# Kernel optimization log

Hardware: AMD Instinct MI355X
Metric: run time of the kernel (lower is better)

## Reference

```python
import jax, jax.numpy as jnp
import numpy as np

N_NODES = 50000
N_EDGES = 800000
D = 128


def setup_inputs() -> dict:
    key = jax.random.key(0)
    k1, k2, k3, k4, k5 = jax.random.split(key, 5)
    feature = jax.random.normal(k1, (N_NODES, D), dtype=jnp.float32)
    src = jax.random.randint(k2, (N_EDGES,), 0, N_NODES, dtype=jnp.int64)
    dst = jax.random.randint(k3, (N_EDGES,), 0, N_NODES, dtype=jnp.int64)
    # Linear(in_feats=128, out_feats=128) params
    W = jax.random.normal(k4, (D, D), dtype=jnp.float32) * (1.0 / np.sqrt(D))
    b = jax.random.normal(k5, (D,), dtype=jnp.float32) * 0.01
    return {"feature": feature, "src": src, "dst": dst, "W": W, "b": b}


def reference(feature, src, dst, W, b):
    n = feature.shape[0]
    # copy_src message: each edge carries h[src]; segment-mean over in-edges at dst
    msgs = feature[src]                                      # [E, D] irregular gather
    summed = jax.ops.segment_sum(msgs, dst, num_segments=n)  # [N, D] scatter-add
    cnt = jax.ops.segment_sum(jnp.ones((src.shape[0],), dtype=feature.dtype),
                              dst, num_segments=n)           # in-degree per node
    h = summed / jnp.clip(cnt, 1.0)[:, None]                 # mean (isolated nodes -> 0)
    # NodeApplyModule: ReLU(W h + b)
    return jax.nn.relu(h @ W.T + b)
```

## Files before the change

kernel.cpp:

```cpp
#include <hip/hip_runtime.h>

#define NN 50000
#define NE 800000
#define DD 128
#define NPAD 50176
#define NSB 49
#define WGB 512
#define HBW 391
#define HB 782


#define ACC4(A, V) { A.x += V.x; A.y += V.y; A.z += V.z; A.w += V.w; }

#define BSUM_PREFIX(bsum, sbase)                                   \
  {                                                                \
    int tt = threadIdx.x;                                          \
    if (tt < 64) {                                                 \
      int b = (tt < NSB) ? bsum[tt] : 0;                           \
      int z = b;                                                   \
      _Pragma("unroll") for (int o = 1; o < 64; o <<= 1) {         \
        int w_ = __shfl_up(z, o);                                  \
        if (tt >= o) z += w_;                                      \
      }                                                            \
      sbase[tt] = z - b;                                           \
    }                                                              \
    __syncthreads();                                               \
  }

__global__ __launch_bounds__(256) void k_gemm_hist(
    const float* __restrict__ feat, const float* __restrict__ W,
    float* __restrict__ g, const int* __restrict__ dst, int* __restrict__ cnt) {
  __shared__ float4 Wc4[DD * 32];
  __shared__ float hs[4][8][DD];
  int tid = threadIdx.x;
  int bid = blockIdx.x;

  if (bid >= WGB) {
    int idx = (bid - WGB) * 256 + tid;
    if (idx < NE / 8) {
      const int4* d4 = (const int4*)dst;
      int4 a = d4[idx * 2];
      int4 b = d4[idx * 2 + 1];
      atomicAdd(&cnt[a.x], 1); atomicAdd(&cnt[a.y], 1);
      atomicAdd(&cnt[a.z], 1); atomicAdd(&cnt[a.w], 1);
      atomicAdd(&cnt[b.x], 1); atomicAdd(&cnt[b.y], 1);
      atomicAdd(&cnt[b.z], 1); atomicAdd(&cnt[b.w], 1);
    }
    return;
  }

  {
    const float4* W4 = (const float4*)W;
#pragma unroll
    for (int i = 0; i < 16; ++i) {
      int fidx = tid + (i << 8);
      int c = fidx >> 5, kq = fidx & 31;
      Wc4[c * 32 + (kq ^ (c & 31))] = W4[fidx];
    }
  }
  __syncthreads();

  int w = tid >> 6, lane = tid & 63;
  int s = lane & 31;
  const float2* feat2 = (const float2*)feat;

  for (int gid = bid * 4 + w; gid < NN / 8; gid += WGB * 4) {
    int r0 = gid * 8;
#pragma unroll
    for (int r = 0; r < 8; ++r) {
      float2 v = feat2[(size_t)(r0 + r) * 64 + lane];
      hs[w][r][lane * 2] = v.x;
      hs[w][r][lane * 2 + 1] = v.y;
    }
    float2 acc[8] = {};
#pragma unroll 2
    for (int kc = 0; kc < 32; ++kc) {
      float4 w0 = Wc4[lane * 32 + (kc ^ s)];
      float4 w1 = Wc4[(lane + 64) * 32 + (kc ^ s)];
#pragma unroll
      for (int r = 0; r < 8; ++r) {
        float4 h = *(const float4*)&hs[w][r][kc * 4];
        acc[r].x += h.x * w0.x; acc[r].x += h.y * w0.y;
        acc[r].x += h.z * w0.z; acc[r].x += h.w * w0.w;
        acc[r].y += h.x * w1.x; acc[r].y += h.y * w1.y;
        acc[r].y += h.z * w1.z; acc[r].y += h.w * w1.w;
      }
    }
#pragma unroll
    for (int r = 0; r < 8; ++r) {
      g[(size_t)(r0 + r) * DD + lane] = acc[r].x;
      g[(size_t)(r0 + r) * DD + lane + 64] = acc[r].y;
    }
  }
}

__global__ __launch_bounds__(1024) void k_scan(const int* __restrict__ cnt,
                                               int* __restrict__ pos,
                                               int* __restrict__ bsum) {
  __shared__ int wsum[16];
  int t = threadIdx.x;
  int gidx = blockIdx.x * 1024 + t;
  int v = cnt[gidx];
  int x = v;
#pragma unroll
  for (int o = 1; o < 64; o <<= 1) {
    int y = __shfl_up(x, o);
    if ((t & 63) >= o) x += y;
  }
  if ((t & 63) == 63) wsum[t >> 6] = x;
  __syncthreads();
  if (t < 64) {
    int y = (t < 16) ? wsum[t] : 0;
    int z = y;
#pragma unroll
    for (int o = 1; o < 16; o <<= 1) {
      int w = __shfl_up(z, o);
      if (t >= o) z += w;
    }
    if (t < 16) wsum[t] = z - y;
  }
  __syncthreads();
  pos[gidx] = wsum[t >> 6] + x - v;
  if (t == 1023) bsum[blockIdx.x] = wsum[15] + x;
}

__global__ __launch_bounds__(256) void k_fill(const int* __restrict__ src,
                                              const int* __restrict__ dst,
                                              int* __restrict__ pos,
                                              int* __restrict__ csr,
                                              const int* __restrict__ bsum) {
  __shared__ int sbase[64];
  BSUM_PREFIX(bsum, sbase)
  int idx = blockIdx.x * 256 + threadIdx.x;
  if (idx < NE / 4) {
    int4 d = ((const int4*)dst)[idx];
    int4 s = ((const int4*)src)[idx];
    int p;
    p = atomicAdd(&pos[d.x], 1); csr[sbase[d.x >> 10] + p] = s.x;
    p = atomicAdd(&pos[d.y], 1); csr[sbase[d.y >> 10] + p] = s.y;
    p = atomicAdd(&pos[d.z], 1); csr[sbase[d.z >> 10] + p] = s.z;
    p = atomicAdd(&pos[d.w], 1); csr[sbase[d.w >> 10] + p] = s.w;
  }
}

__global__ __launch_bounds__(256) void k_gmean(const float* __restrict__ g,
                                               const int* __restrict__ csr,
                                               const int* __restrict__ pos,
                                               const int* __restrict__ cnt,
                                               const int* __restrict__ bsum,
                                               const float* __restrict__ bias,
                                               float* __restrict__ out) {
  __shared__ int sbase[64];
  BSUM_PREFIX(bsum, sbase)
  int tid = threadIdx.x;
  int hw = tid >> 5, l32 = tid & 31;
  int n = blockIdx.x * 8 + hw;
  int c = cnt[n];
  int endg = sbase[n >> 10] + pos[n];
  int start = endg - c;
  float4 a0 = make_float4(0.f, 0.f, 0.f, 0.f), a1 = a0, a2 = a0, a3 = a0;

  for (int base = start; base < endg; base += 32) {
    int m = endg - base;
    if (m > 32) m = 32;
    int s = (l32 < m) ? csr[base + l32] : 0;
    int j = 0;
    for (; j + 8 <= m; j += 8) {
      int s0 = __shfl(s, j + 0, 32), s1 = __shfl(s, j + 1, 32),
          s2 = __shfl(s, j + 2, 32), s3 = __shfl(s, j + 3, 32),
          s4 = __shfl(s, j + 4, 32), s5 = __shfl(s, j + 5, 32),
          s6 = __shfl(s, j + 6, 32), s7 = __shfl(s, j + 7, 32);
      float4 v0 = ((const float4*)(g + (size_t)s0 * DD))[l32];
      float4 v1 = ((const float4*)(g + (size_t)s1 * DD))[l32];
      float4 v2 = ((const float4*)(g + (size_t)s2 * DD))[l32];
      float4 v3 = ((const float4*)(g + (size_t)s3 * DD))[l32];
      float4 v4 = ((const float4*)(g + (size_t)s4 * DD))[l32];
      float4 v5 = ((const float4*)(g + (size_t)s5 * DD))[l32];
      float4 v6 = ((const float4*)(g + (size_t)s6 * DD))[l32];
      float4 v7 = ((const float4*)(g + (size_t)s7 * DD))[l32];
      ACC4(a0, v0) ACC4(a1, v1) ACC4(a2, v2) ACC4(a3, v3)
      ACC4(a0, v4) ACC4(a1, v5) ACC4(a2, v6) ACC4(a3, v7)
    }
    for (; j < m; ++j) {
      int sj = __shfl(s, j, 32);
      float4 v = ((const float4*)(g + (size_t)sj * DD))[l32];
      ACC4(a0, v)
    }
  }
  a0.x += a1.x + a2.x + a3.x;
  a0.y += a1.y + a2.y + a3.y;
  a0.z += a1.z + a2.z + a3.z;
  a0.w += a1.w + a2.w + a3.w;
  float inv = 1.0f / fmaxf((float)c, 1.0f);
  float4 b4 = ((const float4*)bias)[l32];
  float4 o;
  o.x = fmaxf(a0.x * inv + b4.x, 0.f);
  o.y = fmaxf(a0.y * inv + b4.y, 0.f);
  o.z = fmaxf(a0.z * inv + b4.z, 0.f);
  o.w = fmaxf(a0.w * inv + b4.w, 0.f);
  ((float4*)(out + (size_t)n * DD))[l32] = o;
}

__global__ __launch_bounds__(128) void k_hist(const int* __restrict__ dst,
                                              int* __restrict__ cnt) {
  int idx = blockIdx.x * 128 + threadIdx.x;
  if (idx < NE / 8) {
    const int4* d4 = (const int4*)dst;
    int4 a = d4[idx * 2];
    int4 b = d4[idx * 2 + 1];
    atomicAdd(&cnt[a.x], 1); atomicAdd(&cnt[a.y], 1);
    atomicAdd(&cnt[a.z], 1); atomicAdd(&cnt[a.w], 1);
    atomicAdd(&cnt[b.x], 1); atomicAdd(&cnt[b.y], 1);
    atomicAdd(&cnt[b.z], 1); atomicAdd(&cnt[b.w], 1);
  }
}

__global__ __launch_bounds__(256) void k_gsum(const float* __restrict__ feat,
                                              const int* __restrict__ csr,
                                              const int* __restrict__ pos,
                                              const int* __restrict__ cnt,
                                              const int* __restrict__ bsum,
                                              float* __restrict__ out) {
  __shared__ int sbase[64];
  BSUM_PREFIX(bsum, sbase)
  int tid = threadIdx.x;
  int hw = tid >> 5, l32 = tid & 31;
  int n = blockIdx.x * 8 + hw;
  int c = cnt[n];
  int endg = sbase[n >> 10] + pos[n];
  int start = endg - c;
  float4 a0 = make_float4(0.f, 0.f, 0.f, 0.f), a1 = a0;
  for (int base = start; base < endg; base += 32) {
    int m = endg - base;
    if (m > 32) m = 32;
    int s = (l32 < m) ? csr[base + l32] : 0;
    for (int j = 0; j < m; ++j) {
      int sj = __shfl(s, j, 32);
      float4 v = ((const float4*)(feat + (size_t)sj * DD))[l32];
      if (j & 1) { ACC4(a1, v) } else { ACC4(a0, v) }
    }
  }
  a0.x += a1.x; a0.y += a1.y; a0.z += a1.z; a0.w += a1.w;
  ((float4*)(out + (size_t)n * DD))[l32] = a0;
}

__global__ __launch_bounds__(256) void k_gemm_inplace(float* __restrict__ io,
                                                      const int* __restrict__ cnt,
                                                      const float* __restrict__ W,
                                                      const float* __restrict__ bias) {
  __shared__ float Wt[64][132];
  __shared__ __attribute__((aligned(16))) float hs[64][72];
  int tid = threadIdx.x;
  int row0 = blockIdx.x * 64;
  int tc = tid & 31;
  int tr = tid >> 5;
  float acc[8][4] = {};
  for (int p = 0; p < 2; ++p) {
    if (p) __syncthreads();
    for (int i = 0; i < 8; ++i) {
      int fidx = tid + (i << 8);
      int c = fidx >> 4;
      int kq = fidx & 15;
      float4 w = ((const float4*)W)[c * 32 + p * 16 + kq];
      int kk = kq << 2;
      Wt[kk + 0][c ^ (((kk + 0) & 31) << 2)] = w.x;
      Wt[kk + 1][c ^ (((kk + 1) & 31) << 2)] = w.y;
      Wt[kk + 2][c ^ (((kk + 2) & 31) << 2)] = w.z;
      Wt[kk + 3][c ^ (((kk + 3) & 31) << 2)] = w.w;
    }
    for (int i = 0; i < 4; ++i) {
      int fidx = tid + (i << 8);
      int r = fidx & 63;
      int kq = fidx >> 6;
      int grow = row0 + r;
      float4 v = make_float4(0.f, 0.f, 0.f, 0.f);
      if (grow < NN) {
        v = ((const float4*)io)[(size_t)grow * 32 + p * 16 + kq];
        float inv = 1.0f / fmaxf((float)cnt[grow], 1.0f);
        v.x *= inv; v.y *= inv; v.z *= inv; v.w *= inv;
      }
      int kk = kq << 2;
      hs[kk + 0][r] = v.x;
      hs[kk + 1][r] = v.y;
      hs[kk + 2][r] = v.z;
      hs[kk + 3][r] = v.w;
    }
    __syncthreads();
#pragma unroll 4
    for (int kk = 0; kk < 64; ++kk) {
      float4 w4 = *(const float4*)&Wt[kk][(tc << 2) ^ ((kk & 31) << 2)];
      float4 h0 = *(const float4*)&hs[kk][tr << 3];
      float4 h1 = *(const float4*)&hs[kk][(tr << 3) + 4];
      acc[0][0] += h0.x * w4.x; acc[0][1] += h0.x * w4.y; acc[0][2] += h0.x * w4.z; acc[0][3] += h0.x * w4.w;
      acc[1][0] += h0.y * w4.x; acc[1][1] += h0.y * w4.y; acc[1][2] += h0.y * w4.z; acc[1][3] += h0.y * w4.w;
      acc[2][0] += h0.z * w4.x; acc[2][1] += h0.z * w4.y; acc[2][2] += h0.z * w4.z; acc[2][3] += h0.z * w4.w;
      acc[3][0] += h0.w * w4.x; acc[3][1] += h0.w * w4.y; acc[3][2] += h0.w * w4.z; acc[3][3] += h0.w * w4.w;
      acc[4][0] += h1.x * w4.x; acc[4][1] += h1.x * w4.y; acc[4][2] += h1.x * w4.z; acc[4][3] += h1.x * w4.w;
      acc[5][0] += h1.y * w4.x; acc[5][1] += h1.y * w4.y; acc[5][2] += h1.y * w4.z; acc[5][3] += h1.y * w4.w;
      acc[6][0] += h1.z * w4.x; acc[6][1] += h1.z * w4.y; acc[6][2] += h1.z * w4.z; acc[6][3] += h1.z * w4.w;
      acc[7][0] += h1.w * w4.x; acc[7][1] += h1.w * w4.y; acc[7][2] += h1.w * w4.z; acc[7][3] += h1.w * w4.w;
    }
  }
  float4 b4 = ((const float4*)bias)[tc];
#pragma unroll
  for (int r = 0; r < 8; ++r) {
    int row = row0 + (tr << 3) + r;
    if (row < NN) {
      float4 o;
      o.x = fmaxf(acc[r][0] + b4.x, 0.f);
      o.y = fmaxf(acc[r][1] + b4.y, 0.f);
      o.z = fmaxf(acc[r][2] + b4.z, 0.f);
      o.w = fmaxf(acc[r][3] + b4.w, 0.f);
      ((float4*)(io + (size_t)row * DD))[tc] = o;
    }
  }
}

extern "C" void kernel_launch(void* const* d_in, const int* in_sizes, int n_in,
                              void* d_out, int out_size, void* d_ws, size_t ws_size,
                              hipStream_t stream) {
  const float* feature = (const float*)d_in[0];
  const int*   src     = (const int*)d_in[1];
  const int*   dst     = (const int*)d_in[2];
  const float* W       = (const float*)d_in[3];
  const float* bias    = (const float*)d_in[4];
  float* out = (float*)d_out;

  int* cnt  = (int*)d_ws;
  int* pos  = cnt + NPAD;
  int* bsum = pos + NPAD;
  int* csr  = bsum + 64;
  float* g  = (float*)(csr + NE);

  size_t need_main = (size_t)(2 * NPAD + 64 + NE) * 4 + (size_t)NN * DD * 4;

  hipMemsetAsync(cnt, 0, NPAD * sizeof(int), stream);

  if (ws_size >= need_main) {
    hipLaunchKernelGGL(k_gemm_hist, dim3(WGB + HBW), dim3(256), 0, stream,
                       feature, W, g, dst, cnt);
    hipLaunchKernelGGL(k_scan, dim3(NSB), dim3(1024), 0, stream, cnt, pos, bsum);
    hipLaunchKernelGGL(k_fill, dim3((NE / 4 + 255) / 256), dim3(256), 0, stream,
                       src, dst, pos, csr, bsum);
    hipLaunchKernelGGL(k_gmean, dim3(NN / 8), dim3(256), 0, stream,
                       g, csr, pos, cnt, bsum, bias, out);
  } else {
    hipLaunchKernelGGL(k_hist, dim3(HB), dim3(128), 0, stream, dst, cnt);
    hipLaunchKernelGGL(k_scan, dim3(NSB), dim3(1024), 0, stream, cnt, pos, bsum);
    hipLaunchKernelGGL(k_fill, dim3((NE / 4 + 255) / 256), dim3(256), 0, stream,
                       src, dst, pos, csr, bsum);
    hipLaunchKernelGGL(k_gsum, dim3(NN / 8), dim3(256), 0, stream,
                       feature, csr, pos, cnt, bsum, out);
    hipLaunchKernelGGL(k_gemm_inplace, dim3((NN + 63) / 64), dim3(256), 0,
                       stream, out, cnt, W, bias);
  }
}
```

Baseline: 240.3 us.

## Fuse histogram, GEMM, scan, CSR fill and gather-mean into one cooperative kernel

Replaces the memset plus four-kernel pipeline with a single persistent cooperative kernel that uses grid-wide syncs between phases: zeroing counts, histogram plus GEMM, chunked scan, CSR fill, and gather-mean with bias and ReLU. The GEMM is re-partitioned so each block computes a 32-column slice of W, which lets a smaller W tile live in shared memory. The aim is to remove kernel launch gaps and the separate memset. In exchange, each phase is limited to a fixed grid of 1008 blocks, and grid.sync barriers can cost more than a launch boundary. The old multi-kernel path remains as a fallback when cooperative launch is unsupported or fails.

After: 693.1 us. +188.4%, slower.

```diff
diff --git a/kernel.cpp b/kernel.cpp
--- a/kernel.cpp
+++ b/kernel.cpp
@@ -1,9 +1,14 @@
 #include <hip/hip_runtime.h>
+#include <hip/hip_cooperative_groups.h>
+
+namespace cg = cooperative_groups;
 
 #define NN 50000
 #define NE 800000
 #define DD 128
 #define NPAD 50176
+#define NCH 196
+#define CGRID 1008
 #define NSB 49
 #define WGB 512
 #define HBW 391
@@ -27,6 +32,179 @@
     __syncthreads();                                               \
   }
 
+__global__ __launch_bounds__(256, 4) void k_mega(
+    const float* __restrict__ feat, const float* __restrict__ W,
+    const int* __restrict__ src, const int* __restrict__ dst,
+    const float* __restrict__ bias, float* __restrict__ out,
+    int* cnt, int* pos, int* bsum, int* csr, float* g) {
+  __shared__ float4 Wq4[32 * 32];
+  __shared__ __attribute__((aligned(16))) float hs[4][8][DD];
+  __shared__ int wsum[4];
+  __shared__ int sbase[NCH];
+
+  cg::grid_group grid = cg::this_grid();
+  int tid = threadIdx.x;
+  int bid = blockIdx.x;
+  int nb = gridDim.x;
+
+  for (int i = bid * 256 + tid; i < NPAD; i += nb * 256) cnt[i] = 0;
+  grid.sync();
+
+  int cgp = bid & 3;
+  int col0 = cgp * 32;
+  {
+    const float4* W4 = (const float4*)W;
+#pragma unroll
+    for (int i = 0; i < 4; ++i) {
+      int fidx = tid + (i << 8);
+      int c = fidx >> 5, kq = fidx & 31;
+      Wq4[c * 32 + (kq ^ c)] = W4[(size_t)(col0 + c) * 32 + kq];
+    }
+  }
+  for (int idx = bid * 256 + tid; idx < NE / 4; idx += nb * 256) {
+    int4 d = ((const int4*)dst)[idx];
+    atomicAdd(&cnt[d.x], 1); atomicAdd(&cnt[d.y], 1);
+    atomicAdd(&cnt[d.z], 1); atomicAdd(&cnt[d.w], 1);
+  }
+  __syncthreads();
+  {
+    int w = tid >> 6, lane = tid & 63;
+    int hw = lane >> 5, c = lane & 31;
+    const float2* feat2 = (const float2*)feat;
+    for (int gid = (bid >> 2) * 4 + w; gid < NN / 8; gid += (nb >> 2) * 4) {
+      int r0 = gid * 8;
+#pragma unroll
+      for (int r = 0; r < 8; ++r) {
+        float2 v = feat2[(size_t)(r0 + r) * 64 + lane];
+        hs[w][r][lane * 2] = v.x;
+        hs[w][r][lane * 2 + 1] = v.y;
+      }
+      float a0 = 0.f, a1 = 0.f, a2 = 0.f, a3 = 0.f;
+#pragma unroll 4
+      for (int kc = 0; kc < 32; ++kc) {
+        float4 w4 = Wq4[c * 32 + (kc ^ c)];
+        float4 h0 = *(const float4*)&hs[w][hw * 4 + 0][kc * 4];
+        float4 h1 = *(const float4*)&hs[w][hw * 4 + 1][kc * 4];
+        float4 h2 = *(const float4*)&hs[w][hw * 4 + 2][kc * 4];
+        float4 h3 = *(const float4*)&hs[w][hw * 4 + 3][kc * 4];
+        a0 += h0.x * w4.x + h0.y * w4.y + h0.z * w4.z + h0.w * w4.w;
+        a1 += h1.x * w4.x + h1.y * w4.y + h1.z * w4.z + h1.w * w4.w;
+        a2 += h2.x * w4.x + h2.y * w4.y + h2.z * w4.z + h2.w * w4.w;
+        a3 += h3.x * w4.x + h3.y * w4.y + h3.z * w4.z + h3.w * w4.w;
+      }
+      int rb = r0 + hw * 4;
+      g[(size_t)(rb + 0) * DD + col0 + c] = a0;
+      g[(size_t)(rb + 1) * DD + col0 + c] = a1;
+      g[(size_t)(rb + 2) * DD + col0 + c] = a2;
+      g[(size_t)(rb + 3) * DD + col0 + c] = a3;
+    }
+  }
+  grid.sync();
+
+  for (int chunk = bid; chunk < NCH; chunk += nb) {
+    int v = cnt[chunk * 256 + tid];
+    int x = v;
+#pragma unroll
+    for (int o = 1; o < 64; o <<= 1) {
+      int y = __shfl_up(x, o);
+      if ((tid & 63) >= o) x += y;
+    }
+    if ((tid & 63) == 63) wsum[tid >> 6] = x;
+    __syncthreads();
+    if (tid == 0) {
+      int s = 0;
+#pragma unroll
+      for (int i = 0; i < 4; ++i) { int t2 = wsum[i]; wsum[i] = s; s += t2; }
+    }
+    __syncthreads();
+    pos[chunk * 256 + tid] = wsum[tid >> 6] + x - v;
+    if (tid == 255) bsum[chunk] = wsum[3] + x;
+    __syncthreads();
+  }
+  grid.sync();
+
+  if (tid < 64) {
+    int b4[4] = {0, 0, 0, 0};
+    int ssum = 0;
+    if (tid < 49) {
+#pragma unroll
+      for (int i = 0; i < 4; ++i) { b4[i] = bsum[tid * 4 + i]; ssum += b4[i]; }
+    }
+    int z = ssum;
+#pragma unroll
+    for (int o = 1; o < 64; o <<= 1) {
+      int y = __shfl_up(z, o);
+      if (tid >= o) z += y;
+    }
+    int base = z - ssum;
+    if (tid < 49) {
+      int run = base;
+#pragma unroll
+      for (int i = 0; i < 4; ++i) { sbase[tid * 4 + i] = run; run += b4[i]; }
+    }
+  }
+  __syncthreads();
+  for (int idx = bid * 256 + tid; idx < NE / 4; idx += nb * 256) {
+    int4 d = ((const int4*)dst)[idx];
+    int4 s = ((const int4*)src)[idx];
+    int p;
+    p = atomicAdd(&pos[d.x], 1); csr[sbase[d.x >> 8] + p] = s.x;
+    p = atomicAdd(&pos[d.y], 1); csr[sbase[d.y >> 8] + p] = s.y;
+    p = atomicAdd(&pos[d.z], 1); csr[sbase[d.z >> 8] + p] = s.z;
+    p = atomicAdd(&pos[d.w], 1); csr[sbase[d.w >> 8] + p] = s.w;
+  }
+  grid.sync();
+
+  {
+    int hw8 = tid >> 5, l32 = tid & 31;
+    for (int n = bid * 8 + hw8; n < NN; n += nb * 8) {
+      int c = cnt[n];
+      int endg = sbase[n >> 8] + pos[n];
+      int start = endg - c;
+      float4 a0 = make_float4(0.f, 0.f, 0.f, 0.f), a1 = a0, a2 = a0, a3 = a0;
+      for (int base = start; base < endg; base += 32) {
+        int m = endg - base;
+        if (m > 32) m = 32;
+        int s = (l32 < m) ? csr[base + l32] : 0;
+        int j = 0;
+        for (; j + 8 <= m; j += 8) {
+          int s0 = __shfl(s, j + 0, 32), s1 = __shfl(s, j + 1, 32),
+              s2 = __shfl(s, j + 2, 32), s3 = __shfl(s, j + 3, 32),
+              s4 = __shfl(s, j + 4, 32), s5 = __shfl(s, j + 5, 32),
+              s6 = __shfl(s, j + 6, 32), s7 = __shfl(s, j + 7, 32);
+          float4 v0 = ((const float4*)(g + (size_t)s0 * DD))[l32];
+          float4 v1 = ((const float4*)(g + (size_t)s1 * DD))[l32];
+          float4 v2 = ((const float4*)(g + (size_t)s2 * DD))[l32];
+          float4 v3 = ((const float4*)(g + (size_t)s3 * DD))[l32];
+          float4 v4 = ((const float4*)(g + (size_t)s4 * DD))[l32];
+          float4 v5 = ((const float4*)(g + (size_t)s5 * DD))[l32];
+          float4 v6 = ((const float4*)(g + (size_t)s6 * DD))[l32];
+          float4 v7 = ((const float4*)(g + (size_t)s7 * DD))[l32];
+          ACC4(a0, v0) ACC4(a1, v1) ACC4(a2, v2) ACC4(a3, v3)
+          ACC4(a0, v4) ACC4(a1, v5) ACC4(a2, v6) ACC4(a3, v7)
+        }
+        for (; j < m; ++j) {
+          int sj = __shfl(s, j, 32);
+          float4 v = ((const float4*)(g + (size_t)sj * DD))[l32];
+          ACC4(a0, v)
+        }
+      }
+      a0.x += a1.x + a2.x + a3.x;
+      a0.y += a1.y + a2.y + a3.y;
+      a0.z += a1.z + a2.z + a3.z;
+      a0.w += a1.w + a2.w + a3.w;
+      float inv = 1.0f / fmaxf((float)c, 1.0f);
+      float4 b4 = ((const float4*)bias)[l32];
+      float4 o;
+      o.x = fmaxf(a0.x * inv + b4.x, 0.f);
+      o.y = fmaxf(a0.y * inv + b4.y, 0.f);
+      o.z = fmaxf(a0.z * inv + b4.z, 0.f);
+      o.w = fmaxf(a0.w * inv + b4.w, 0.f);
+      ((float4*)(out + (size_t)n * DD))[l32] = o;
+    }
+  }
+}
+
 __global__ __launch_bounds__(256) void k_gemm_hist(
     const float* __restrict__ feat, const float* __restrict__ W,
     float* __restrict__ g, const int* __restrict__ dst, int* __restrict__ cnt) {
@@ -48,7 +226,6 @@
     }
     return;
   }
-
   {
     const float4* W4 = (const float4*)W;
 #pragma unroll
@@ -59,11 +236,9 @@
     }
   }
   __syncthreads();
-
   int w = tid >> 6, lane = tid & 63;
   int s = lane & 31;
   const float2* feat2 = (const float2*)feat;
-
   for (int gid = bid * 4 + w; gid < NN / 8; gid += WGB * 4) {
     int r0 = gid * 8;
 #pragma unroll
@@ -159,7 +334,6 @@
   int endg = sbase[n >> 10] + pos[n];
   int start = endg - c;
   float4 a0 = make_float4(0.f, 0.f, 0.f, 0.f), a1 = a0, a2 = a0, a3 = a0;
-
   for (int base = start; base < endg; base += 32) {
     int m = endg - base;
     if (m > 32) m = 32;
@@ -329,13 +503,25 @@
   int* cnt  = (int*)d_ws;
   int* pos  = cnt + NPAD;
   int* bsum = pos + NPAD;
-  int* csr  = bsum + 64;
+  int* csr  = bsum + 256;
   float* g  = (float*)(csr + NE);
 
-  size_t need_main = (size_t)(2 * NPAD + 64 + NE) * 4 + (size_t)NN * DD * 4;
+  size_t need_main = (size_t)(2 * NPAD + 256 + NE) * 4 + (size_t)NN * DD * 4;
+
+  int coop = 0, dev = 0;
+  hipGetDevice(&dev);
+  hipDeviceGetAttribute(&coop, hipDeviceAttributeCooperativeLaunch, dev);
+
+  if (coop && ws_size >= need_main) {
+    void* args[] = {(void*)&feature, (void*)&W, (void*)&src, (void*)&dst,
+                    (void*)&bias, (void*)&out, (void*)&cnt, (void*)&pos,
+                    (void*)&bsum, (void*)&csr, (void*)&g};
+    hipError_t e = hipLaunchCooperativeKernel((const void*)k_mega, dim3(CGRID),
+                                              dim3(256), args, 0, stream);
+    if (e == hipSuccess) return;
+  }
 
   hipMemsetAsync(cnt, 0, NPAD * sizeof(int), stream);
-
   if (ws_size >= need_main) {
     hipLaunchKernelGGL(k_gemm_hist, dim3(WGB + HBW), dim3(256), 0, stream,
                        feature, W, g, dst, cnt);
```
